# Kernel optimization log

Measured on AMD Instinct MI355X. Metric: run time of the kernel, lower is better.

## Reference

```python
import jax, jax.numpy as jnp
import numpy as np

D_MODEL = 512
NUM_HEADS = 8
DEPTH = D_MODEL // NUM_HEADS
PROJ_DIM = 256
SEQ_LEN = 4096
BATCH = 8


def _glorot(key, shape):
    fan_in, fan_out = shape[-2], shape[-1]
    limit = np.sqrt(6.0 / (fan_in + fan_out))
    return jax.random.uniform(key, shape, jnp.float32, -limit, limit)


def setup_inputs() -> dict:
    key = jax.random.key(0)
    ks = jax.random.split(key, 8)
    x = jax.random.normal(ks[0], (BATCH, SEQ_LEN, D_MODEL), jnp.float32)
    wq = _glorot(ks[1], (D_MODEL, D_MODEL))
    wk = _glorot(ks[2], (D_MODEL, D_MODEL))
    wv = _glorot(ks[3], (D_MODEL, D_MODEL))
    E = _glorot(ks[4], (NUM_HEADS, SEQ_LEN, PROJ_DIM))
    F = _glorot(ks[5], (NUM_HEADS, SEQ_LEN, PROJ_DIM))
    w_out = _glorot(ks[6], (D_MODEL, D_MODEL))
    b_out = jnp.zeros((D_MODEL,), jnp.float32)
    return {"x": x, "wq": wq, "wk": wk, "wv": wv, "E": E, "F": F,
            "w_out": w_out, "b_out": b_out}


def reference(x, wq, wk, wv, E, F, w_out, b_out):
    b, n, _ = x.shape
    # QKV projections + split heads -> [b, h, n, d]
    def split_heads(t):
        return t.reshape(b, n, NUM_HEADS, DEPTH).transpose(0, 2, 1, 3)
    q = split_heads(x @ wq)
    k = split_heads(x @ wk)
    v = split_heads(x @ wv)
    # Linformer low-rank projection of K/V along sequence: [b,h,r,d]
    k_proj = jnp.einsum('bhnd,hnr->bhrd', k, E)
    v_proj = jnp.einsum('bhnd,hnr->bhrd', v, F)
    scale = 1.0 / jnp.sqrt(jnp.asarray(DEPTH, jnp.float32))
    scores = jnp.einsum('bhnd,bhrd->bhnr', q, k_proj) * scale  # [b,h,n,r]
    attn = jax.nn.softmax(scores, axis=-1)
    out = jnp.einsum('bhnr,bhrd->bhnd', attn, v_proj)
    out = out.transpose(0, 2, 1, 3).reshape(b, n, D_MODEL)
    return out @ w_out + b_out
```

## Files before the change

kernel.cpp:

```cpp
#include <hip/hip_runtime.h>

typedef unsigned short u16;
typedef unsigned int   u32;
typedef __bf16 bf16x8 __attribute__((ext_vector_type(8)));
typedef float  f32x4  __attribute__((ext_vector_type(4)));
typedef u16    u16x4  __attribute__((ext_vector_type(4)));

#define DEV __device__ __forceinline__

DEV u16 f2bf(float f) {
    u32 u = __builtin_bit_cast(u32, f);
    u = (u + 0x7fffu + ((u >> 16) & 1u)) >> 16;
    return (u16)u;
}

DEV void gload16(const void* g, void* l) {
    __builtin_amdgcn_global_load_lds((const __attribute__((address_space(1))) u32*)g,
                                     (__attribute__((address_space(3))) u32*)l, 16, 0, 0);
}

__global__ __launch_bounds__(256) void k_prep(const float* __restrict__ x,
                                              const float* __restrict__ wq, const float* __restrict__ wk,
                                              const float* __restrict__ wv, const float* __restrict__ wo,
                                              const float* __restrict__ E, const float* __restrict__ F,
                                              u16* __restrict__ xb, u16* __restrict__ wcatT, u16* __restrict__ woT,
                                              u16* __restrict__ Et, u16* __restrict__ Ft) {
    __shared__ u16 tile[64][65];
    const int t = threadIdx.x;
    const int bid = blockIdx.x;
    if (bid < 16384) {
        int i = (bid * 256 + t) * 4;
        float4 v = *(const float4*)(x + i);
        u16x4 o;
        o[0] = f2bf(v.x); o[1] = f2bf(v.y); o[2] = f2bf(v.z); o[3] = f2bf(v.w);
        *(u16x4*)(xb + i) = o;
    } else if (bid < 20480) {
        const int b2 = bid - 16384;
        const int rt = b2 & 3, ntl = (b2 >> 2) & 63, h = (b2 >> 8) & 7, which = b2 >> 11;
        const float* src = (which ? F : E) + (size_t)h * 4096 * 256;
        u16* dst = (which ? Ft : Et) + (size_t)h * 256 * 4096;
        const int n0 = ntl * 64, r0 = rt * 64;
#pragma unroll
        for (int it = 0; it < 16; ++it) {
            const int idx = t + it * 256;
            const int nl = idx >> 6, rl = idx & 63;
            tile[nl][rl] = f2bf(src[(size_t)(n0 + nl) * 256 + r0 + rl]);
        }
        __syncthreads();
#pragma unroll
        for (int it = 0; it < 16; ++it) {
            const int idx = t + it * 256;
            const int rl = idx >> 6, nl = idx & 63;
            dst[(size_t)(r0 + rl) * 4096 + n0 + nl] = tile[nl][rl];
        }
    } else {
        const int b2 = bid - 20480;
        const int mi = b2 >> 6, tix = b2 & 63;
        const int jt = tix & 7, kt = tix >> 3;
        const float* w = (mi == 0) ? wq : (mi == 1) ? wk : (mi == 2) ? wv : wo;
        u16* dst = (mi < 3) ? (wcatT + mi * 262144) : woT;
#pragma unroll
        for (int it = 0; it < 16; ++it) {
            const int idx = t + it * 256;
            const int kl = idx >> 6, jl = idx & 63;
            tile[kl][jl] = f2bf(w[(kt * 64 + kl) * 512 + jt * 64 + jl]);
        }
        __syncthreads();
#pragma unroll
        for (int it = 0; it < 16; ++it) {
            const int idx = t + it * 256;
            const int jl = idx >> 6, kl = idx & 63;
            dst[(size_t)(jt * 64 + jl) * 512 + kt * 64 + kl] = tile[kl][jl];
        }
    }
}

template <int MODE>
__global__ __launch_bounds__(256) void k_gemm(const u16* __restrict__ A, const u16* __restrict__ Bm,
                                              u16* __restrict__ Qo, u16* __restrict__ Kt, u16* __restrict__ Vt,
                                              float* __restrict__ Of, const float* __restrict__ bias,
                                              int M, int N, int K) {
    __shared__ __attribute__((aligned(16))) char smem[32768];
    const int tid = threadIdx.x;
    const int lane = tid & 63, wid = tid >> 6;
    const int wr = wid >> 1, wc = wid & 1;
    const int g = lane >> 4, l16 = lane & 15;
    const int bid = (int)blockIdx.x;
    const int xcd = bid & 7, loc = bid >> 3;
    const int bm = xcd * 32 + (loc & 31), bn = loc >> 5;
    const int m0 = bm << 7, n0 = bn << 7;

    f32x4 acc[4][4] = {};

    for (int k0 = 0; k0 < K; k0 += 64) {
#pragma unroll
        for (int c = 0; c < 4; ++c) {
            const int off = c * 4096 + tid * 16;
            const int row = off >> 7;
            const int sc = ((off >> 4) & 7) ^ (row & 7);
            gload16(A  + (size_t)(m0 + row) * K + (k0 + sc * 8), smem + off);
            gload16(Bm + (size_t)(n0 + row) * K + (k0 + sc * 8), smem + 16384 + off);
        }
        __syncthreads();
#pragma unroll
        for (int kk = 0; kk < 64; kk += 32) {
            bf16x8 av[4], bv[4];
#pragma unroll
            for (int m = 0; m < 4; ++m) {
                const int r = wr * 64 + m * 16 + l16;
                av[m] = *(const bf16x8*)(smem + r * 128 + ((kk * 2 + g * 16) ^ ((r & 7) << 4)));
            }
#pragma unroll
            for (int n = 0; n < 4; ++n) {
                const int r = wc * 64 + n * 16 + l16;
                bv[n] = *(const bf16x8*)(smem + 16384 + r * 128 + ((kk * 2 + g * 16) ^ ((r & 7) << 4)));
            }
            __builtin_amdgcn_s_setprio(1);
#pragma unroll
            for (int m = 0; m < 4; ++m)
#pragma unroll
                for (int n = 0; n < 4; ++n)
                    acc[m][n] = __builtin_amdgcn_mfma_f32_16x16x32_bf16(av[m], bv[n], acc[m][n], 0, 0, 0);
            __builtin_amdgcn_s_setprio(0);
        }
        __syncthreads();
    }

    if (MODE == 0) {
        if (n0 < 512) {
#pragma unroll
            for (int m = 0; m < 4; ++m)
#pragma unroll
                for (int n = 0; n < 4; ++n) {
                    const int col = n0 + wc * 64 + n * 16 + l16;
#pragma unroll
                    for (int i = 0; i < 4; ++i) {
                        const int row = m0 + wr * 64 + m * 16 + g * 4 + i;
                        Qo[(size_t)row * 512 + col] = f2bf(acc[m][n][i]);
                    }
                }
        } else {
            u16* dst = (n0 < 1024) ? Kt : Vt;
#pragma unroll
            for (int m = 0; m < 4; ++m)
#pragma unroll
                for (int n = 0; n < 4; ++n) {
                    const int col = (n0 + wc * 64 + n * 16 + l16) & 511;
                    const int h = col >> 6, d = col & 63;
                    const int rowb = m0 + wr * 64 + m * 16 + g * 4;
                    const int b = rowb >> 12, nn = rowb & 4095;
                    u16x4 pk;
#pragma unroll
                    for (int i = 0; i < 4; ++i) pk[i] = f2bf(acc[m][n][i]);
                    *(u16x4*)(dst + ((size_t)((b * 8 + h) * 64 + d)) * 4096 + nn) = pk;
                }
        }
    } else {
#pragma unroll
        for (int m = 0; m < 4; ++m)
#pragma unroll
            for (int n = 0; n < 4; ++n) {
                const int col = n0 + wc * 64 + n * 16 + l16;
                const float bb = bias[col];
#pragma unroll
                for (int i = 0; i < 4; ++i) {
                    const int row = m0 + wr * 64 + m * 16 + g * 4 + i;
                    Of[(size_t)row * N + col] = acc[m][n][i] + bb;
                }
            }
    }
}

__global__ __launch_bounds__(256) void k_proj(const u16* __restrict__ Et, const u16* __restrict__ Ft,
                                              const u16* __restrict__ Kt, const u16* __restrict__ Vt,
                                              float* __restrict__ pbuf) {
    __shared__ __attribute__((aligned(16))) char smem[24576];
    const int tid = threadIdx.x;
    const int lane = tid & 63, wid = tid >> 6;
    const int wr = wid >> 1, wc = wid & 1;
    const int g = lane >> 4, l16 = lane & 15;
    const int bid = blockIdx.x;
    const int sp = bid >> 8, rest = bid & 255;
    const int mt = rest & 1, which = (rest >> 1) & 1, bh = rest >> 2;
    const int h = bh & 7;
    const u16* Ap = (which ? Ft : Et) + (size_t)h * 256 * 4096 + (size_t)mt * 128 * 4096;
    const u16* Bp = (which ? Vt : Kt) + (size_t)bh * 64 * 4096;

    f32x4 acc[4][2] = {};

    const int kbeg = sp * 1024;
    for (int k0 = kbeg; k0 < kbeg + 1024; k0 += 64) {
#pragma unroll
        for (int c = 0; c < 4; ++c) {
            const int off = c * 4096 + tid * 16;
            const int row = off >> 7;
            const int sc = ((off >> 4) & 7) ^ (row & 7);
            gload16(Ap + (size_t)row * 4096 + (k0 + sc * 8), smem + off);
            if (c < 2)
                gload16(Bp + (size_t)row * 4096 + (k0 + sc * 8), smem + 16384 + off);
        }
        __syncthreads();
#pragma unroll
        for (int kk = 0; kk < 64; kk += 32) {
            bf16x8 av[4], bv[2];
#pragma unroll
            for (int m = 0; m < 4; ++m) {
                const int r = wr * 64 + m * 16 + l16;
                av[m] = *(const bf16x8*)(smem + r * 128 + ((kk * 2 + g * 16) ^ ((r & 7) << 4)));
            }
#pragma unroll
            for (int n = 0; n < 2; ++n) {
                const int r = wc * 32 + n * 16 + l16;
                bv[n] = *(const bf16x8*)(smem + 16384 + r * 128 + ((kk * 2 + g * 16) ^ ((r & 7) << 4)));
            }
            __builtin_amdgcn_s_setprio(1);
#pragma unroll
            for (int m = 0; m < 4; ++m)
#pragma unroll
                for (int n = 0; n < 2; ++n)
                    acc[m][n] = __builtin_amdgcn_mfma_f32_16x16x32_bf16(av[m], bv[n], acc[m][n], 0, 0, 0);
            __builtin_amdgcn_s_setprio(0);
        }
        __syncthreads();
    }

    float* pb = pbuf + ((size_t)(sp * 2 + which) * 64 + bh) * 16384;
    if (which == 0) {
#pragma unroll
        for (int m = 0; m < 4; ++m)
#pragma unroll
            for (int n = 0; n < 2; ++n) {
                const int d = wc * 32 + n * 16 + l16;
#pragma unroll
                for (int i = 0; i < 4; ++i) {
                    const int rg = mt * 128 + wr * 64 + m * 16 + g * 4 + i;
                    pb[rg * 64 + d] = acc[m][n][i];
                }
            }
    } else {
#pragma unroll
        for (int m = 0; m < 4; ++m)
#pragma unroll
            for (int n = 0; n < 2; ++n) {
                const int d = wc * 32 + n * 16 + l16;
                const int r4 = mt * 128 + wr * 64 + m * 16 + g * 4;
                *(f32x4*)(pb + d * 256 + r4) = acc[m][n];
            }
    }
}

__global__ __launch_bounds__(256) void k_preduce(const float* __restrict__ pbuf, u16* __restrict__ outkv) {
    const int o = ((int)blockIdx.x * 256 + (int)threadIdx.x) * 4;
    f32x4 s = *(const f32x4*)(pbuf + o);
    s += *(const f32x4*)(pbuf + 2097152 + o);
    s += *(const f32x4*)(pbuf + 4194304 + o);
    s += *(const f32x4*)(pbuf + 6291456 + o);
    u16x4 r;
#pragma unroll
    for (int i = 0; i < 4; ++i) r[i] = f2bf(s[i]);
    *(u16x4*)(outkv + o) = r;
}

__global__ __launch_bounds__(256) void k_flash(const u16* __restrict__ Q, const u16* __restrict__ kp,
                                               const u16* __restrict__ vpT, u16* __restrict__ ctx) {
    __shared__ __attribute__((aligned(16))) char smem[65536];
    const int tid = threadIdx.x;
    const int lane = tid & 63, w = tid >> 6;
    const int g = lane >> 4, l16 = lane & 15;
    const int bid = blockIdx.x;
    const int nt = bid & 63, bh = bid >> 6;
    const int b = bh >> 3, h = bh & 7;
    const int n0 = nt * 64;

#pragma unroll
    for (int c = 0; c < 8; ++c) {
        const int off = c * 4096 + tid * 16;
        {
            const int row = off >> 7;
            const int sc = ((off >> 4) & 7) ^ (row & 7);
            gload16(kp + (size_t)bh * 16384 + row * 64 + sc * 8, smem + off);
        }
        {
            const int row = off >> 9;
            const int sc = ((off >> 4) & 31) ^ (row & 7);
            gload16(vpT + (size_t)bh * 16384 + row * 256 + sc * 8, smem + 32768 + off);
        }
    }
    const size_t qbase = (size_t)(b * 4096 + n0 + w * 16 + l16) * 512 + h * 64 + g * 8;
    bf16x8 qf0 = *(const bf16x8*)(Q + qbase);
    bf16x8 qf1 = *(const bf16x8*)(Q + qbase + 32);
    __syncthreads();

    f32x4 s[16];
    __builtin_amdgcn_s_setprio(1);
#pragma unroll
    for (int rt = 0; rt < 16; ++rt) {
        const int r = rt * 16 + l16;
        const int sw = (r & 7) << 4;
        bf16x8 kv0 = *(const bf16x8*)(smem + r * 128 + ((g * 16) ^ sw));
        bf16x8 kv1 = *(const bf16x8*)(smem + r * 128 + ((64 + g * 16) ^ sw));
        f32x4 z = {0.f, 0.f, 0.f, 0.f};
        z = __builtin_amdgcn_mfma_f32_16x16x32_bf16(qf0, kv0, z, 0, 0, 0);
        z = __builtin_amdgcn_mfma_f32_16x16x32_bf16(qf1, kv1, z, 0, 0, 0);
        s[rt] = z;
    }
    __builtin_amdgcn_s_setprio(0);

    float mx[4] = {-1e30f, -1e30f, -1e30f, -1e30f};
#pragma unroll
    for (int rt = 0; rt < 16; ++rt)
#pragma unroll
        for (int i = 0; i < 4; ++i) {
            s[rt][i] *= 0.125f;
            mx[i] = fmaxf(mx[i], s[rt][i]);
        }
#pragma unroll
    for (int i = 0; i < 4; ++i) {
        mx[i] = fmaxf(mx[i], __shfl_xor(mx[i], 1));
        mx[i] = fmaxf(mx[i], __shfl_xor(mx[i], 2));
        mx[i] = fmaxf(mx[i], __shfl_xor(mx[i], 4));
        mx[i] = fmaxf(mx[i], __shfl_xor(mx[i], 8));
    }
    float sm[4] = {0.f, 0.f, 0.f, 0.f};
#pragma unroll
    for (int rt = 0; rt < 16; ++rt)
#pragma unroll
        for (int i = 0; i < 4; ++i) {
            float e = __expf(s[rt][i] - mx[i]);
            s[rt][i] = e;
            sm[i] += e;
        }
#pragma unroll
    for (int i = 0; i < 4; ++i) {
        sm[i] += __shfl_xor(sm[i], 1);
        sm[i] += __shfl_xor(sm[i], 2);
        sm[i] += __shfl_xor(sm[i], 4);
        sm[i] += __shfl_xor(sm[i], 8);
    }

    __syncthreads();

#pragma unroll
    for (int rt = 0; rt < 16; ++rt)
#pragma unroll
        for (int i = 0; i < 4; ++i) {
            const int nrow = g * 4 + i;
            const int byte = w * 8192 + nrow * 512 + ((rt * 32 + l16 * 2) ^ ((nrow & 7) << 4));
            *(u16*)(smem + byte) = f2bf(s[rt][i]);
        }
    bf16x8 af[8];
#pragma unroll
    for (int ks = 0; ks < 8; ++ks) {
        const int byte = w * 8192 + l16 * 512 + ((ks * 64 + g * 16) ^ ((l16 & 7) << 4));
        af[ks] = *(const bf16x8*)(smem + byte);
    }
    f32x4 o[4] = {};
    __builtin_amdgcn_s_setprio(1);
#pragma unroll
    for (int dt = 0; dt < 4; ++dt)
#pragma unroll
        for (int ks = 0; ks < 8; ++ks) {
            const int row = dt * 16 + l16;
            const int byte = 32768 + row * 512 + ((ks * 64 + g * 16) ^ ((row & 7) << 4));
            bf16x8 bv = *(const bf16x8*)(smem + byte);
            o[dt] = __builtin_amdgcn_mfma_f32_16x16x32_bf16(af[ks], bv, o[dt], 0, 0, 0);
        }
    __builtin_amdgcn_s_setprio(0);
    float rinv[4];
#pragma unroll
    for (int i = 0; i < 4; ++i) rinv[i] = 1.0f / sm[i];
#pragma unroll
    for (int dt = 0; dt < 4; ++dt)
#pragma unroll
        for (int i = 0; i < 4; ++i) {
            const int row = b * 4096 + n0 + w * 16 + g * 4 + i;
            const int col = h * 64 + dt * 16 + l16;
            ctx[(size_t)row * 512 + col] = f2bf(o[dt][i] * rinv[i]);
        }
}


extern "C" void kernel_launch(void* const* d_in, const int* in_sizes, int n_in,
                              void* d_out, int out_size, void* d_ws, size_t ws_size,
                              hipStream_t stream) {
    const float* x  = (const float*)d_in[0];
    const float* wq = (const float*)d_in[1];
    const float* wk = (const float*)d_in[2];
    const float* wv = (const float*)d_in[3];
    const float* E  = (const float*)d_in[4];
    const float* F  = (const float*)d_in[5];
    const float* wo = (const float*)d_in[6];
    const float* bo = (const float*)d_in[7];
    float* out = (float*)d_out;
    u16* ws = (u16*)d_ws;

    u16* xb    = ws;
    u16* Qm    = ws + 16777216;
    u16* Kt    = ws + 33554432;
    u16* Vt    = ws + 50331648;
    u16* Et    = ws + 67108864;
    u16* Ft    = ws + 75497472;
    u16* wcatT = ws + 83886080;
    u16* woT   = ws + 84672512;
    u16* kpB   = ws + 84934656;
    u16* vpT   = ws + 85983232;
    float* pbuf = (float*)xb;
    u16* ctx   = xb;

    k_prep<<<20736, 256, 0, stream>>>(x, wq, wk, wv, wo, E, F, xb, wcatT, woT, Et, Ft);
    k_gemm<0><<<3072, 256, 0, stream>>>(xb, wcatT, Qm, Kt, Vt, nullptr, nullptr, 32768, 1536, 512);
    k_proj<<<1024, 256, 0, stream>>>(Et, Ft, Kt, Vt, pbuf);
    k_preduce<<<2048, 256, 0, stream>>>(pbuf, kpB);
    k_flash<<<4096, 256, 0, stream>>>(Qm, kpB, vpT, ctx);
    k_gemm<1><<<1024, 256, 0, stream>>>(ctx, woT, nullptr, nullptr, nullptr, out, bo, 32768, 512, 512);
}
```

Baseline: 385.3 us.

## Replace GEMM with 256x256-tile 8-wave kernel and multi-stage async LDS pipeline

Rewrites the QKV and output-projection GEMM as a 512-thread kernel that computes 256x256 tiles. Operands are staged into a 4-slot, 128 KB LDS ring using direct global-to-LDS loads, with explicit vmcnt waits so that loads for later k-halves overlap the MFMA work. Tiles are assigned to blocks in per-XCD contiguous chunks. The aim is more reuse per byte loaded and hidden memory latency, at the cost of fewer blocks (768 and 256), a large LDS footprint, and hand-tuned wait counts that must match the number of loads in flight.

```diff
diff --git a/kernel.cpp b/kernel.cpp
--- a/kernel.cpp
+++ b/kernel.cpp
@@ -17,6 +17,15 @@
 DEV void gload16(const void* g, void* l) {
     __builtin_amdgcn_global_load_lds((const __attribute__((address_space(1))) u32*)g,
                                      (__attribute__((address_space(3))) u32*)l, 16, 0, 0);
+}
+
+DEV void vmw(int n) {
+    switch (n) {
+        case 0:  asm volatile("s_waitcnt vmcnt(0)" ::: "memory"); break;
+        case 4:  asm volatile("s_waitcnt vmcnt(4)" ::: "memory"); break;
+        case 8:  asm volatile("s_waitcnt vmcnt(8)" ::: "memory"); break;
+        default: asm volatile("s_waitcnt vmcnt(10)" ::: "memory"); break;
+    }
 }
 
 __global__ __launch_bounds__(256) void k_prep(const float* __restrict__ x,
@@ -76,96 +85,133 @@
 }
 
 template <int MODE>
-__global__ __launch_bounds__(256) void k_gemm(const u16* __restrict__ A, const u16* __restrict__ Bm,
-                                              u16* __restrict__ Qo, u16* __restrict__ Kt, u16* __restrict__ Vt,
-                                              float* __restrict__ Of, const float* __restrict__ bias,
-                                              int M, int N, int K) {
-    __shared__ __attribute__((aligned(16))) char smem[32768];
+__global__ __launch_bounds__(512, 2) void k_gemm8(const u16* __restrict__ A, const u16* __restrict__ Bm,
+                                                  u16* __restrict__ Qo, u16* __restrict__ Kt, u16* __restrict__ Vt,
+                                                  float* __restrict__ Of, const float* __restrict__ bias,
+                                                  int M, int N, int K) {
+    __shared__ __attribute__((aligned(16))) char smem[131072];
     const int tid = threadIdx.x;
-    const int lane = tid & 63, wid = tid >> 6;
-    const int wr = wid >> 1, wc = wid & 1;
+    const int lane = tid & 63, w = tid >> 6;
+    const int wr = w >> 2, wcn = w & 3;
     const int g = lane >> 4, l16 = lane & 15;
+    const int nbm = M >> 8;
+    const int total = nbm * (N >> 8);
+    const int chunk = total >> 3;
     const int bid = (int)blockIdx.x;
-    const int xcd = bid & 7, loc = bid >> 3;
-    const int bm = xcd * 32 + (loc & 31), bn = loc >> 5;
-    const int m0 = bm << 7, n0 = bn << 7;
-
-    f32x4 acc[4][4] = {};
-
-    for (int k0 = 0; k0 < K; k0 += 64) {
-#pragma unroll
-        for (int c = 0; c < 4; ++c) {
-            const int off = c * 4096 + tid * 16;
-            const int row = off >> 7;
-            const int sc = ((off >> 4) & 7) ^ (row & 7);
-            gload16(A  + (size_t)(m0 + row) * K + (k0 + sc * 8), smem + off);
-            gload16(Bm + (size_t)(n0 + row) * K + (k0 + sc * 8), smem + 16384 + off);
-        }
-        __syncthreads();
-#pragma unroll
-        for (int kk = 0; kk < 64; kk += 32) {
-            bf16x8 av[4], bv[4];
-#pragma unroll
-            for (int m = 0; m < 4; ++m) {
-                const int r = wr * 64 + m * 16 + l16;
-                av[m] = *(const bf16x8*)(smem + r * 128 + ((kk * 2 + g * 16) ^ ((r & 7) << 4)));
-            }
-#pragma unroll
-            for (int n = 0; n < 4; ++n) {
-                const int r = wc * 64 + n * 16 + l16;
-                bv[n] = *(const bf16x8*)(smem + 16384 + r * 128 + ((kk * 2 + g * 16) ^ ((r & 7) << 4)));
-            }
+    const int tt = (bid & 7) * chunk + (bid >> 3);
+    const int bm = tt % nbm, bn = tt / nbm;
+    const int m0 = bm << 8, n0 = bn << 8;
+    const int NT = K >> 6;
+
+    auto stage_h = [&](int h) {
+        const int ktile = h >> 2, ty = h & 3;
+        const int kh = ty >> 1;
+        const int isB = ty & 1;
+        const int slot = (ktile * 2 + kh) & 3;
+        const u16* src = isB ? Bm : A;
+        const int r0 = isB ? n0 : m0;
+        char* base = smem + isB * 65536 + slot * 16384;
+#pragma unroll
+        for (int j = 0; j < 2; ++j) {
+            const int off = j * 8192 + tid * 16;
+            const int row = off >> 6, c = (off >> 4) & 3;
+            const int sc = c ^ ((row >> 1) & 3);
+            gload16(src + (size_t)(r0 + row) * K + ktile * 64 + kh * 32 + sc * 8, base + off);
+        }
+    };
+
+    for (int h = 0; h < 6; ++h) stage_h(h);
+    vmw(8);
+    __builtin_amdgcn_sched_barrier(0);
+    __builtin_amdgcn_s_barrier();
+
+    f32x4 acc[8][4] = {};
+    bf16x8 av[8];
+    for (int kt = 0; kt < NT; ++kt) {
+#pragma unroll
+        for (int s = 0; s < 4; ++s) {
+            const int kh = s >> 1, nh = s & 1;
+            const int slot = (kt * 2 + kh) & 3;
+            char* abase = smem + slot * 16384;
+            char* bbase = smem + 65536 + slot * 16384;
+            if (nh == 0) {
+#pragma unroll
+                for (int m = 0; m < 8; ++m) {
+                    const int row = wr * 128 + m * 16 + l16;
+                    const int c = g ^ ((row >> 1) & 3);
+                    av[m] = *(const bf16x8*)(abase + row * 64 + c * 16);
+                }
+            }
+            bf16x8 bv[2];
+#pragma unroll
+            for (int n = 0; n < 2; ++n) {
+                const int col = wcn * 64 + nh * 32 + n * 16 + l16;
+                const int c = g ^ ((col >> 1) & 3);
+                bv[n] = *(const bf16x8*)(bbase + col * 64 + c * 16);
+            }
+            const int hst = kt * 4 + s + 6;
+            if (hst < NT * 4) stage_h(hst);
             __builtin_amdgcn_s_setprio(1);
 #pragma unroll
-            for (int m = 0; m < 4; ++m)
-#pragma unroll
-                for (int n = 0; n < 4; ++n)
-                    acc[m][n] = __builtin_amdgcn_mfma_f32_16x16x32_bf16(av[m], bv[n], acc[m][n], 0, 0, 0);
+            for (int m = 0; m < 8; ++m)
+#pragma unroll
+                for (int n = 0; n < 2; ++n)
+                    acc[m][nh * 2 + n] = __builtin_amdgcn_mfma_f32_16x16x32_bf16(av[m], bv[n], acc[m][nh * 2 + n], 0, 0, 0);
             __builtin_amdgcn_s_setprio(0);
-        }
-        __syncthreads();
+            const bool last = (kt == NT - 1) && (s == 3);
+            if (!last) {
+                int n;
+                if (s == 0)      n = (kt < NT - 1) ? 10 : 4;
+                else if (s == 1) n = (kt < NT - 1) ? 8 : 0;
+                else if (s == 2) n = (kt < NT - 2) ? 10 : ((kt == NT - 2) ? 8 : 0);
+                else             n = (kt < NT - 2) ? 8 : 4;
+                vmw(n);
+                __builtin_amdgcn_sched_barrier(0);
+                __builtin_amdgcn_s_barrier();
+            }
+        }
     }
 
     if (MODE == 0) {
         if (n0 < 512) {
 #pragma unroll
-            for (int m = 0; m < 4; ++m)
-#pragma unroll
-                for (int n = 0; n < 4; ++n) {
-                    const int col = n0 + wc * 64 + n * 16 + l16;
+            for (int m = 0; m < 8; ++m)
+#pragma unroll
+                for (int jn = 0; jn < 4; ++jn) {
+                    const int col = n0 + wcn * 64 + jn * 16 + l16;
 #pragma unroll
                     for (int i = 0; i < 4; ++i) {
-                        const int row = m0 + wr * 64 + m * 16 + g * 4 + i;
-                        Qo[(size_t)row * 512 + col] = f2bf(acc[m][n][i]);
+                        const int row = m0 + wr * 128 + m * 16 + g * 4 + i;
+                        Qo[(size_t)row * 512 + col] = f2bf(acc[m][jn][i]);
                     }
                 }
         } else {
             u16* dst = (n0 < 1024) ? Kt : Vt;
 #pragma unroll
-            for (int m = 0; m < 4; ++m)
-#pragma unroll
-                for (int n = 0; n < 4; ++n) {
-                    const int col = (n0 + wc * 64 + n * 16 + l16) & 511;
+            for (int m = 0; m < 8; ++m)
+#pragma unroll
+                for (int jn = 0; jn < 4; ++jn) {
+                    const int col = (n0 + wcn * 64 + jn * 16 + l16) & 511;
                     const int h = col >> 6, d = col & 63;
-                    const int rowb = m0 + wr * 64 + m * 16 + g * 4;
+                    const int rowb = m0 + wr * 128 + m * 16 + g * 4;
                     const int b = rowb >> 12, nn = rowb & 4095;
                     u16x4 pk;
 #pragma unroll
-                    for (int i = 0; i < 4; ++i) pk[i] = f2bf(acc[m][n][i]);
+                    for (int i = 0; i < 4; ++i) pk[i] = f2bf(acc[m][jn][i]);
                     *(u16x4*)(dst + ((size_t)((b * 8 + h) * 64 + d)) * 4096 + nn) = pk;
                 }
         }
     } else {
 #pragma unroll
-        for (int m = 0; m < 4; ++m)
-#pragma unroll
-            for (int n = 0; n < 4; ++n) {
-                const int col = n0 + wc * 64 + n * 16 + l16;
+        for (int m = 0; m < 8; ++m)
+#pragma unroll
+            for (int jn = 0; jn < 4; ++jn) {
+                const int col = n0 + wcn * 64 + jn * 16 + l16;
                 const float bb = bias[col];
 #pragma unroll
                 for (int i = 0; i < 4; ++i) {
-                    const int row = m0 + wr * 64 + m * 16 + g * 4 + i;
-                    Of[(size_t)row * N + col] = acc[m][n][i] + bb;
+                    const int row = m0 + wr * 128 + m * 16 + g * 4 + i;
+                    Of[(size_t)row * N + col] = acc[m][jn][i] + bb;
                 }
             }
     }
@@ -408,9 +454,9 @@
     u16* ctx   = xb;
 
     k_prep<<<20736, 256, 0, stream>>>(x, wq, wk, wv, wo, E, F, xb, wcatT, woT, Et, Ft);
-    k_gemm<0><<<3072, 256, 0, stream>>>(xb, wcatT, Qm, Kt, Vt, nullptr, nullptr, 32768, 1536, 512);
+    k_gemm8<0><<<768, 512, 0, stream>>>(xb, wcatT, Qm, Kt, Vt, nullptr, nullptr, 32768, 1536, 512);
     k_proj<<<1024, 256, 0, stream>>>(Et, Ft, Kt, Vt, pbuf);
     k_preduce<<<2048, 256, 0, stream>>>(pbuf, kpB);
     k_flash<<<4096, 256, 0, stream>>>(Qm, kpB, vpT, ctx);
-    k_gemm<1><<<1024, 256, 0, stream>>>(ctx, woT, nullptr, nullptr, nullptr, out, bo, 32768, 512, 512);
-}
+    k_gemm8<1><<<256, 512, 0, stream>>>(ctx, woT, nullptr, nullptr, nullptr, out, bo, 32768, 512, 512);
+}
```

Result: no change. 379.6 us (-1.5%).
